# Performance work log

Measured on AMD Instinct MI355X. Metric: run time of the kernel, lower is better.

## Reference

```python
import jax, jax.numpy as jnp
import numpy as np

QMAX = 127.0
QMIN = -128.0


def setup_inputs() -> dict:
    key = jax.random.key(0)
    k1, k2, k3 = jax.random.split(key, 3)
    B, N, D, O = 4, 4096, 2048, 2048
    x = jax.random.normal(k1, (B, N, D), dtype=jnp.float32)
    weight = jax.random.normal(k2, (O, D), dtype=jnp.float32)
    bias = jax.random.normal(k3, (O,), dtype=jnp.float32)
    return {"x": x, "weight": weight, "bias": bias}


def reference(x, weight, bias):
    # --- per-row symmetric int8 quantization of the weight [O, D] ---
    w_max = jnp.clip(jnp.max(jnp.abs(weight), axis=1, keepdims=True), 1e-8, None)
    w_scale = (w_max / QMAX)                     # [O, 1]
    w_q = jnp.clip(jnp.round(weight / w_scale), QMIN, QMAX).astype(jnp.int8)
    w_scale = w_scale.squeeze(1).astype(jnp.float32)  # [O]

    # --- dynamic per-row symmetric int8 quantization of x [B, N, D] ---
    x_max = jnp.max(jnp.abs(x), axis=2, keepdims=True)       # [B, N, 1]
    x_scale = jnp.maximum(x_max / QMAX, 1e-12)               # [B, N, 1]
    x_q = jnp.clip(jnp.round(x / x_scale), QMIN, QMAX).astype(jnp.int8)

    # --- int8 GEMM accumulated in int32: [B,N,D] x [O,D]^T -> [B,N,O] ---
    acc = jnp.einsum("bnd,od->bno", x_q.astype(jnp.int32), w_q.astype(jnp.int32))

    # --- dequantize with per-row activation scale and per-out-channel weight scale ---
    y = acc.astype(jnp.float32) * x_scale.astype(jnp.float32) * w_scale[None, None, :]
    y = y + bias
    return y.astype(x.dtype)
```

## Files before the change

### kernel.cpp

```cpp
#include <hip/hip_runtime.h>
#include <stdint.h>
#include <stddef.h>

typedef int v4i __attribute__((ext_vector_type(4)));

#define GLOAD_LDS16(g, l) __builtin_amdgcn_global_load_lds( \
    (const __attribute__((address_space(1))) void*)(g),     \
    (__attribute__((address_space(3))) void*)(l), 16, 0, 0)

__device__ __forceinline__ int pack4(float4 f, float s) {
    int a = (int)rintf(f.x / s); a = a < -128 ? -128 : (a > 127 ? 127 : a);
    int b = (int)rintf(f.y / s); b = b < -128 ? -128 : (b > 127 ? 127 : b);
    int c = (int)rintf(f.z / s); c = c < -128 ? -128 : (c > 127 ? 127 : c);
    int d = (int)rintf(f.w / s); d = d < -128 ? -128 : (d > 127 ? 127 : d);
    return (a & 255) | ((b & 255) << 8) | ((c & 255) << 16) | ((d & 255) << 24);
}

__global__ __launch_bounds__(256) void quant_rows_2048(
    const float* __restrict__ in, signed char* __restrict__ q,
    float* __restrict__ scales, float floorv)
{
    const int lane = threadIdx.x & 63;
    const int row  = blockIdx.x * 4 + (threadIdx.x >> 6);
    const float* rp = in + (size_t)row * 2048;

    float4 v[8];
#pragma unroll
    for (int j = 0; j < 2; ++j) {
        const float4* p = (const float4*)(rp + j * 1024 + lane * 16);
#pragma unroll
        for (int i = 0; i < 4; ++i) v[j * 4 + i] = p[i];
    }
    float am = 0.0f;
#pragma unroll
    for (int i = 0; i < 8; ++i) {
        am = fmaxf(am, fabsf(v[i].x));
        am = fmaxf(am, fabsf(v[i].y));
        am = fmaxf(am, fabsf(v[i].z));
        am = fmaxf(am, fabsf(v[i].w));
    }
#pragma unroll
    for (int off = 32; off; off >>= 1) am = fmaxf(am, __shfl_xor(am, off));
    const float s = fmaxf(am / 127.0f, floorv);

#pragma unroll
    for (int j = 0; j < 2; ++j) {
        int4 pk;
        pk.x = pack4(v[j * 4 + 0], s);
        pk.y = pack4(v[j * 4 + 1], s);
        pk.z = pack4(v[j * 4 + 2], s);
        pk.w = pack4(v[j * 4 + 3], s);
        *(int4*)(q + (size_t)row * 2048 + j * 1024 + lane * 16) = pk;
    }
    if (lane == 0) scales[row] = s;
}

__global__ __launch_bounds__(512, 4) void gemm_i8_occ(
    const signed char* __restrict__ xq, const signed char* __restrict__ wq,
    const float* __restrict__ xs, const float* __restrict__ ws,
    const float* __restrict__ bias, float* __restrict__ out, int K)
{
    __shared__ __align__(16) signed char lds[49152];

    const int tid  = threadIdx.x;
    const int lane = tid & 63;
    const int wid  = tid >> 6;
    const int wm   = wid >> 2;
    const int wn   = wid & 3;

    const int nwg  = gridDim.x * gridDim.y;
    int orig = blockIdx.y * gridDim.x + blockIdx.x;
    int swz  = ((nwg & 7) == 0) ? ((orig & 7) * (nwg >> 3) + (orig >> 3)) : orig;
    const int brow = (swz / gridDim.x) * 128;
    const int bcol = (swz % gridDim.x) * 256;

    const int gch  = (((tid & 3) ^ ((tid >> 3) & 3)) << 4);
    const int lofs = tid << 4;
    const signed char* gA  = xq + (size_t)(brow + (tid >> 2)) * K;
    const signed char* gB0 = wq + (size_t)(bcol + (tid >> 2)) * K;
    const signed char* gB1 = wq + (size_t)(bcol + 128 + (tid >> 2)) * K;

#define ST_A(tt, bb)  GLOAD_LDS16(gA  + (size_t)(tt) * 64 + gch, lds + ((bb) ? 8192 : 0) + lofs)
#define ST_B0(tt, bb) GLOAD_LDS16(gB0 + (size_t)(tt) * 64 + gch, lds + 16384 + ((bb) ? 16384 : 0) + lofs)
#define ST_B1(tt, bb) GLOAD_LDS16(gB1 + (size_t)(tt) * 64 + gch, lds + 24576 + ((bb) ? 16384 : 0) + lofs)

    const int rl   = lane & 15;
    const int ko   = lane >> 4;
    const int slot = ((ko ^ ((rl >> 1) & 3)) << 4);

#define FRAG_A(bb, r) (*(const v4i*)(lds + (((bb) ? 8192 : 0) + (r) * 64 + slot)))
#define FRAG_B(bb, r) (*(const v4i*)(lds + (16384 + ((bb) ? 16384 : 0) + (r) * 64 + slot)))

    v4i acc[4][4] = {};
    const int ar = wm * 64 + rl;
    const int br = wn * 64 + rl;

    ST_A(0, 0); ST_B0(0, 0); ST_B1(0, 0);
    __syncthreads();

    const int NT = K >> 6;
    for (int t = 0; t < NT; ++t) {
        const int buf = t & 1;
        if (t + 1 < NT) {
            ST_A(t + 1, buf ^ 1);
            ST_B0(t + 1, buf ^ 1);
            ST_B1(t + 1, buf ^ 1);
        }
        v4i af[4], bf[4];
#pragma unroll
        for (int m = 0; m < 4; ++m) af[m] = FRAG_A(buf, ar + m * 16);
#pragma unroll
        for (int n = 0; n < 4; ++n) bf[n] = FRAG_B(buf, br + n * 16);
#pragma unroll
        for (int m = 0; m < 4; ++m)
#pragma unroll
            for (int n = 0; n < 4; ++n)
                acc[m][n] = __builtin_amdgcn_mfma_i32_16x16x64_i8(
                    af[m], bf[n], acc[m][n], 0, 0, 0);
        __syncthreads();
    }

    const int rg = lane >> 4;
#pragma unroll
    for (int n = 0; n < 4; ++n) {
        const int col = bcol + wn * 64 + n * 16 + rl;
        const float wsc = ws[col];
        const float bv  = bias[col];
#pragma unroll
        for (int m = 0; m < 4; ++m) {
#pragma unroll
            for (int j = 0; j < 4; ++j) {
                const int row = brow + wm * 64 + m * 16 + rg * 4 + j;
                out[(size_t)row * 2048 + col] =
                    (float)acc[m][n][j] * xs[row] * wsc + bv;
            }
        }
    }
#undef ST_A
#undef ST_B0
#undef ST_B1
#undef FRAG_A
#undef FRAG_B
}

extern "C" void kernel_launch(void* const* d_in, const int* in_sizes, int n_in,
                              void* d_out, int out_size, void* d_ws, size_t ws_size,
                              hipStream_t stream) {
    const float* x    = (const float*)d_in[0];
    const float* w    = (const float*)d_in[1];
    const float* bias = (const float*)d_in[2];
    float* out = (float*)d_out;

    const int D = 2048;
    const int O = in_sizes[2];
    const int M = in_sizes[0] / D;

    char* wsb = (char*)d_ws;
    signed char* xq  = (signed char*)wsb;
    signed char* wqp = (signed char*)(wsb + (size_t)M * D);
    float* xs  = (float*)(wsb + (size_t)M * D + (size_t)O * D);
    float* wsc = (float*)(wsb + (size_t)M * D + (size_t)O * D + (size_t)M * 4);

    quant_rows_2048<<<M / 4, 256, 0, stream>>>(x, xq, xs, 1e-12f);
    quant_rows_2048<<<O / 4, 256, 0, stream>>>(w, wqp, wsc, 1e-8f / 127.0f);

    dim3 grid(O / 256, M / 128);
    gemm_i8_occ<<<grid, 512, 0, stream>>>(xq, wqp, xs, wsc, bias, out, D);
}
```

Before: 126.4 us.

## Load GEMM B fragments directly from global into registers, bypassing LDS

Replaces the LDS staging of the weight tile with per-wave direct global loads of B fragments into registers, double-buffered across k iterations. LDS usage drops to the A tile only. This removes LDS writes/reads for B but duplicates B global traffic across waves sharing columns and exposes global latency with strided, less coalesced accesses.

```diff
diff --git a/kernel.cpp b/kernel.cpp
--- a/kernel.cpp
+++ b/kernel.cpp
@@ -55,12 +55,12 @@
     if (lane == 0) scales[row] = s;
 }
 
-__global__ __launch_bounds__(512, 4) void gemm_i8_occ(
+__global__ __launch_bounds__(512, 4) void gemm_i8_breg(
     const signed char* __restrict__ xq, const signed char* __restrict__ wq,
     const float* __restrict__ xs, const float* __restrict__ ws,
     const float* __restrict__ bias, float* __restrict__ out, int K)
 {
-    __shared__ __align__(16) signed char lds[49152];
+    __shared__ __align__(16) signed char lds[16384];
 
     const int tid  = threadIdx.x;
     const int lane = tid & 63;
@@ -76,48 +76,54 @@
 
     const int gch  = (((tid & 3) ^ ((tid >> 3) & 3)) << 4);
     const int lofs = tid << 4;
-    const signed char* gA  = xq + (size_t)(brow + (tid >> 2)) * K;
-    const signed char* gB0 = wq + (size_t)(bcol + (tid >> 2)) * K;
-    const signed char* gB1 = wq + (size_t)(bcol + 128 + (tid >> 2)) * K;
+    const signed char* gA = xq + (size_t)(brow + (tid >> 2)) * K;
 
-#define ST_A(tt, bb)  GLOAD_LDS16(gA  + (size_t)(tt) * 64 + gch, lds + ((bb) ? 8192 : 0) + lofs)
-#define ST_B0(tt, bb) GLOAD_LDS16(gB0 + (size_t)(tt) * 64 + gch, lds + 16384 + ((bb) ? 16384 : 0) + lofs)
-#define ST_B1(tt, bb) GLOAD_LDS16(gB1 + (size_t)(tt) * 64 + gch, lds + 24576 + ((bb) ? 16384 : 0) + lofs)
+#define ST_A(tt, bb) GLOAD_LDS16(gA + (size_t)(tt) * 64 + gch, \
+                                 lds + ((bb) ? 8192 : 0) + lofs)
 
     const int rl   = lane & 15;
     const int ko   = lane >> 4;
     const int slot = ((ko ^ ((rl >> 1) & 3)) << 4);
 
 #define FRAG_A(bb, r) (*(const v4i*)(lds + (((bb) ? 8192 : 0) + (r) * 64 + slot)))
-#define FRAG_B(bb, r) (*(const v4i*)(lds + (16384 + ((bb) ? 16384 : 0) + (r) * 64 + slot)))
+
+    const signed char* gB = wq + (size_t)(bcol + wn * 64 + rl) * K + (ko << 4);
+    const size_t bfs = (size_t)16 * K;
 
     v4i acc[4][4] = {};
     const int ar = wm * 64 + rl;
-    const int br = wn * 64 + rl;
 
-    ST_A(0, 0); ST_B0(0, 0); ST_B1(0, 0);
+    ST_A(0, 0);
+    v4i bc0 = *(const v4i*)(gB);
+    v4i bc1 = *(const v4i*)(gB + bfs);
+    v4i bc2 = *(const v4i*)(gB + 2 * bfs);
+    v4i bc3 = *(const v4i*)(gB + 3 * bfs);
     __syncthreads();
 
     const int NT = K >> 6;
     for (int t = 0; t < NT; ++t) {
         const int buf = t & 1;
+        v4i bn0, bn1, bn2, bn3;
         if (t + 1 < NT) {
             ST_A(t + 1, buf ^ 1);
-            ST_B0(t + 1, buf ^ 1);
-            ST_B1(t + 1, buf ^ 1);
+            const signed char* gBt = gB + (size_t)(t + 1) * 64;
+            bn0 = *(const v4i*)(gBt);
+            bn1 = *(const v4i*)(gBt + bfs);
+            bn2 = *(const v4i*)(gBt + 2 * bfs);
+            bn3 = *(const v4i*)(gBt + 3 * bfs);
         }
-        v4i af[4], bf[4];
+        v4i af[4];
 #pragma unroll
         for (int m = 0; m < 4; ++m) af[m] = FRAG_A(buf, ar + m * 16);
 #pragma unroll
-        for (int n = 0; n < 4; ++n) bf[n] = FRAG_B(buf, br + n * 16);
-#pragma unroll
-        for (int m = 0; m < 4; ++m)
-#pragma unroll
-            for (int n = 0; n < 4; ++n)
-                acc[m][n] = __builtin_amdgcn_mfma_i32_16x16x64_i8(
-                    af[m], bf[n], acc[m][n], 0, 0, 0);
+        for (int m = 0; m < 4; ++m) {
+            acc[m][0] = __builtin_amdgcn_mfma_i32_16x16x64_i8(af[m], bc0, acc[m][0], 0, 0, 0);
+            acc[m][1] = __builtin_amdgcn_mfma_i32_16x16x64_i8(af[m], bc1, acc[m][1], 0, 0, 0);
+            acc[m][2] = __builtin_amdgcn_mfma_i32_16x16x64_i8(af[m], bc2, acc[m][2], 0, 0, 0);
+            acc[m][3] = __builtin_amdgcn_mfma_i32_16x16x64_i8(af[m], bc3, acc[m][3], 0, 0, 0);
+        }
         __syncthreads();
+        if (t + 1 < NT) { bc0 = bn0; bc1 = bn1; bc2 = bn2; bc3 = bn3; }
     }
 
     const int rg = lane >> 4;
@@ -137,10 +143,7 @@
         }
     }
 #undef ST_A
-#undef ST_B0
-#undef ST_B1
 #undef FRAG_A
-#undef FRAG_B
 }
 
 extern "C" void kernel_launch(void* const* d_in, const int* in_sizes, int n_in,
@@ -165,5 +168,5 @@
     quant_rows_2048<<<O / 4, 256, 0, stream>>>(w, wqp, wsc, 1e-8f / 127.0f);
 
     dim3 grid(O / 256, M / 128);
-    gemm_i8_occ<<<grid, 512, 0, stream>>>(xq, wqp, xs, wsc, bias, out, D);
+    gemm_i8_breg<<<grid, 512, 0, stream>>>(xq, wqp, xs, wsc, bias, out, D);
 }
```

Result: slower. 197.7 us (+56.4%).

## Use a three-stage LDS ring buffer with explicit vmcnt waits in int8 GEMM

Applied to the files above, without the earlier changes.

Replaces the double-buffered K loop with a triple-buffered LDS ring that prefetches two tiles ahead. Fine-grained s_waitcnt vmcnt(3) plus raw s_barrier replace __syncthreads, so the next tile's loads can stay in flight across the barrier. MFMA issue is also wrapped in s_setprio to favour the math waves. LDS per block grows from 48KB to 72KB, which may lower the number of resident workgroups per CU below the launch-bounds target.

```diff
diff --git a/kernel.cpp b/kernel.cpp
--- a/kernel.cpp
+++ b/kernel.cpp
@@ -55,12 +55,12 @@
     if (lane == 0) scales[row] = s;
 }
 
-__global__ __launch_bounds__(512, 4) void gemm_i8_occ(
+__global__ __launch_bounds__(512, 4) void gemm_i8_ring(
     const signed char* __restrict__ xq, const signed char* __restrict__ wq,
     const float* __restrict__ xs, const float* __restrict__ ws,
     const float* __restrict__ bias, float* __restrict__ out, int K)
 {
-    __shared__ __align__(16) signed char lds[49152];
+    __shared__ __align__(16) signed char lds[73728];
 
     const int tid  = threadIdx.x;
     const int lane = tid & 63;
@@ -80,44 +80,55 @@
     const signed char* gB0 = wq + (size_t)(bcol + (tid >> 2)) * K;
     const signed char* gB1 = wq + (size_t)(bcol + 128 + (tid >> 2)) * K;
 
-#define ST_A(tt, bb)  GLOAD_LDS16(gA  + (size_t)(tt) * 64 + gch, lds + ((bb) ? 8192 : 0) + lofs)
-#define ST_B0(tt, bb) GLOAD_LDS16(gB0 + (size_t)(tt) * 64 + gch, lds + 16384 + ((bb) ? 16384 : 0) + lofs)
-#define ST_B1(tt, bb) GLOAD_LDS16(gB1 + (size_t)(tt) * 64 + gch, lds + 24576 + ((bb) ? 16384 : 0) + lofs)
+#define BUFOFF(bb) ((bb) * 24576)
+#define ST3(tt, bb) do {                                                         \
+    GLOAD_LDS16(gA  + (size_t)(tt) * 64 + gch, lds + BUFOFF(bb) + lofs);         \
+    GLOAD_LDS16(gB0 + (size_t)(tt) * 64 + gch, lds + BUFOFF(bb) + 8192 + lofs);  \
+    GLOAD_LDS16(gB1 + (size_t)(tt) * 64 + gch, lds + BUFOFF(bb) + 16384 + lofs); \
+} while (0)
 
     const int rl   = lane & 15;
     const int ko   = lane >> 4;
     const int slot = ((ko ^ ((rl >> 1) & 3)) << 4);
 
-#define FRAG_A(bb, r) (*(const v4i*)(lds + (((bb) ? 8192 : 0) + (r) * 64 + slot)))
-#define FRAG_B(bb, r) (*(const v4i*)(lds + (16384 + ((bb) ? 16384 : 0) + (r) * 64 + slot)))
+#define FRAG_A(bb, r) (*(const v4i*)(lds + BUFOFF(bb) + (r) * 64 + slot))
+#define FRAG_B(bb, r) (*(const v4i*)(lds + BUFOFF(bb) + 8192 + (r) * 64 + slot))
 
     v4i acc[4][4] = {};
     const int ar = wm * 64 + rl;
     const int br = wn * 64 + rl;
 
-    ST_A(0, 0); ST_B0(0, 0); ST_B1(0, 0);
-    __syncthreads();
+    ST3(0, 0);
+    ST3(1, 1);
+    asm volatile("s_waitcnt vmcnt(3)" ::: "memory");
+    __builtin_amdgcn_s_barrier();
 
     const int NT = K >> 6;
     for (int t = 0; t < NT; ++t) {
-        const int buf = t & 1;
-        if (t + 1 < NT) {
-            ST_A(t + 1, buf ^ 1);
-            ST_B0(t + 1, buf ^ 1);
-            ST_B1(t + 1, buf ^ 1);
-        }
+        const int buf = t % 3;
+        if (t + 2 < NT) ST3(t + 2, (t + 2) % 3);
+
         v4i af[4], bf[4];
 #pragma unroll
         for (int m = 0; m < 4; ++m) af[m] = FRAG_A(buf, ar + m * 16);
 #pragma unroll
         for (int n = 0; n < 4; ++n) bf[n] = FRAG_B(buf, br + n * 16);
+        __builtin_amdgcn_s_setprio(1);
 #pragma unroll
         for (int m = 0; m < 4; ++m)
 #pragma unroll
             for (int n = 0; n < 4; ++n)
                 acc[m][n] = __builtin_amdgcn_mfma_i32_16x16x64_i8(
                     af[m], bf[n], acc[m][n], 0, 0, 0);
-        __syncthreads();
+        __builtin_amdgcn_s_setprio(0);
+
+        if (t + 2 < NT) {
+            asm volatile("s_waitcnt vmcnt(3) lgkmcnt(0)" ::: "memory");
+            __builtin_amdgcn_s_barrier();
+        } else if (t + 2 == NT) {
+            asm volatile("s_waitcnt vmcnt(0) lgkmcnt(0)" ::: "memory");
+            __builtin_amdgcn_s_barrier();
+        }
     }
 
     const int rg = lane >> 4;
@@ -136,9 +147,8 @@
             }
         }
     }
-#undef ST_A
-#undef ST_B0
-#undef ST_B1
+#undef ST3
+#undef BUFOFF
 #undef FRAG_A
 #undef FRAG_B
 }
@@ -165,5 +175,5 @@
     quant_rows_2048<<<O / 4, 256, 0, stream>>>(w, wqp, wsc, 1e-8f / 127.0f);
 
     dim3 grid(O / 256, M / 128);
-    gemm_i8_occ<<<grid, 512, 0, stream>>>(xq, wqp, xs, wsc, bias, out, D);
+    gemm_i8_ring<<<grid, 512, 0, stream>>>(xq, wqp, xs, wsc, bias, out, D);
 }
```

After: 126.4 us. Within noise of the previous version (+0.0%).
